# Optimization experiments

Hardware: AMD Instinct MI355X
Metric: run time of the kernel (lower is better)

The kernel has to match this reference:

```python
import jax, jax.numpy as jnp
import numpy as np

D_MODEL = 1024
NUM_HEADS = 16
ROPE_THETA = 10000.0


def setup_inputs() -> dict:
    key = jax.random.key(0)
    ks = jax.random.split(key, 5)
    B, S, D = 4, 2048, D_MODEL
    std = (2.0 / (D * D)) ** 0.5
    return {
        "x": jax.random.normal(ks[0], (B, S, D), dtype=jnp.float32),
        "Wq": jax.random.normal(ks[1], (D, D), dtype=jnp.float32) * std,
        "Wk": jax.random.normal(ks[2], (D, D), dtype=jnp.float32) * std,
        "Wv": jax.random.normal(ks[3], (D, D), dtype=jnp.float32) * std,
        "Wo": jax.random.normal(ks[4], (D, D), dtype=jnp.float32) * std,
    }


def _apply_rope(t, sin, cos):
    # t: [B, H, S, d_k]; sin/cos: [S, d_k//2] (broadcast over B, H)
    e = t[..., 0::2]
    o = t[..., 1::2]
    rot = jnp.stack((e * cos - o * sin, e * sin + o * cos), axis=-1)
    return rot.reshape(t.shape)  # interleave back to d_k


def reference(x, Wq, Wk, Wv, Wo):
    B, S, D = x.shape
    H = NUM_HEADS
    dk = D // H

    def proj(W):
        y = jnp.einsum('bsd,ed->bse', x, W)  # Linear: weight is [out, in]
        return y.reshape(B, S, H, dk).transpose(0, 2, 1, 3)  # [B,H,S,dk]

    q, k, v = proj(Wq), proj(Wk), proj(Wv)

    # RoPE cache (token_positions = arange(S))
    half = dk // 2
    inv_freq = 1.0 / (ROPE_THETA ** (jnp.arange(half, dtype=jnp.float32) * 2.0 / dk))
    angles = jnp.arange(S, dtype=jnp.float32)[:, None] * inv_freq[None, :]  # [S, half]
    sin, cos = jnp.sin(angles), jnp.cos(angles)
    q = _apply_rope(q, sin, cos)
    k = _apply_rope(k, sin, cos)

    # scaled dot-product attention with causal mask
    scores = jnp.einsum('bhqd,bhkd->bhqk', q, k) / jnp.sqrt(jnp.float32(dk))
    causal = jnp.tril(jnp.ones((S, S), dtype=bool))
    scores = jnp.where(causal, scores, jnp.finfo(scores.dtype).min)
    p = jax.nn.softmax(scores, axis=-1)
    out = jnp.einsum('bhqk,bhkd->bhqd', p, v)  # [B,H,S,dk]

    out = out.transpose(0, 2, 1, 3).reshape(B, S, D)
    return jnp.einsum('bsd,ed->bse', out, Wo)
```

## Files before the change

kernel.cpp:

```cpp
#include <hip/hip_runtime.h>

typedef unsigned short u16;
typedef unsigned int   u32;

typedef short    short8 __attribute__((ext_vector_type(8)));
typedef __bf16   bf16x8 __attribute__((ext_vector_type(8)));
typedef _Float16 half8  __attribute__((ext_vector_type(8)));
typedef float    f32x4  __attribute__((ext_vector_type(4)));

#define S_LEN   2048
#define DM      1024
#define NHEAD   16
#define DK      64
#define BH_TOT  64
#define M_TOK   8192
#define KDIM    1024

__device__ __forceinline__ u16 f2bf(float f) {
    u32 u = __builtin_bit_cast(u32, f);
    u += 0x7FFFu + ((u >> 16) & 1u);
    return (u16)(u >> 16);
}
__device__ __forceinline__ f32x4 mfma_bf16(short8 a, short8 b, f32x4 c) {
    return __builtin_amdgcn_mfma_f32_16x16x32_bf16(
        __builtin_bit_cast(bf16x8, a), __builtin_bit_cast(bf16x8, b), c, 0, 0, 0);
}
__device__ __forceinline__ f32x4 mfma_f16(half8 a, half8 b, f32x4 c) {
    return __builtin_amdgcn_mfma_f32_16x16x32_f16(a, b, c, 0, 0, 0);
}
__device__ __forceinline__ u32 pk_f16(float a, float b) {
    return __builtin_bit_cast(u32, __builtin_amdgcn_cvt_pkrtz(a, b));
}
__device__ __forceinline__ void gl_lds16(const void* g, void* l) {
    __builtin_amdgcn_global_load_lds(
        (const __attribute__((address_space(1))) u32*)g,
        (__attribute__((address_space(3))) u32*)l, 16, 0, 0);
}
__device__ __forceinline__ void bar_raw() { asm volatile("s_barrier" ::: "memory"); }
__device__ __forceinline__ void wait_vm4() { asm volatile("s_waitcnt vmcnt(4)" ::: "memory"); }
__device__ __forceinline__ void wait_vm0() { asm volatile("s_waitcnt vmcnt(0)" ::: "memory"); }

__device__ __forceinline__ int perm_inv(int rc) {
    const int nt = rc >> 4, mid = (rc >> 2) & 3, r = rc & 3;
    return 32 * (nt >> 1) + 8 * mid + 4 * (nt & 1) + r;
}

__global__ void cvt_all(const float4* __restrict__ x,  const float4* __restrict__ Wq,
                        const float4* __restrict__ Wk, const float4* __restrict__ Wv,
                        const float4* __restrict__ Wo,
                        uint2* __restrict__ oX, uint2* __restrict__ oWcat,
                        uint2* __restrict__ oWo,
                        float* __restrict__ sT, float* __restrict__ cT) {
    const int i = blockIdx.x * 256 + threadIdx.x;
    if (i < 3145728) {
        const float4* in;
        uint2* out;
        if (i < 2097152) {
            in = x + i;  out = oX + i;
        } else {
            const int j = i - 2097152;
            const int w = j >> 18, k = j & 262143;
            in  = (w == 0 ? Wq : w == 1 ? Wk : w == 2 ? Wv : Wo) + k;
            out = (w < 3) ? (oWcat + w * 262144 + k) : (oWo + k);
        }
        float4 f = *in;
        uint2 o;
        o.x = (u32)f2bf(f.x) | ((u32)f2bf(f.y) << 16);
        o.y = (u32)f2bf(f.z) | ((u32)f2bf(f.w) << 16);
        *out = o;
    } else {
        const int idx = i - 3145728;
        const float fi = expf(-(float)(idx >> 11) * 0.287823136624255f);
        const float ang = (float)(idx & 2047) * fi;
        sT[idx] = sinf(ang);
        cT[idx] = cosf(ang);
    }
}

template <int MODE>
__global__ __launch_bounds__(256)
void gemm_nt(const u16* __restrict__ A, const u16* __restrict__ Bw,
             u16* __restrict__ oQ, u16* __restrict__ oK, u16* __restrict__ oVt,
             float* __restrict__ oF,
             const float* __restrict__ ropeS, const float* __restrict__ ropeC) {
    __shared__ u16 As[2][128 * 32];
    __shared__ u16 Bs[2][128 * 32];
    const int tid  = threadIdx.x;
    const int wave = tid >> 6, lane = tid & 63;
    const int quad = lane >> 4, l15 = lane & 15;
    const int wr = wave >> 1, wc = wave & 1;
    const int NX  = (MODE == 0) ? 24 : 8;
    const int lin = (int)blockIdx.x + NX * (int)blockIdx.y;
    const int xcd = lin & 7, idx = lin >> 3;
    const int mbase = (xcd * 8 + idx / NX) * 128;
    const int nbase = (idx % NX) * 128;

    f32x4 acc[4][4];
#pragma unroll
    for (int i = 0; i < 4; i++)
#pragma unroll
        for (int j = 0; j < 4; j++) acc[i][j] = (f32x4)0.0f;

    const int srow0 = wave * 32 + (lane >> 2);
    const int srow1 = srow0 + 16;
    const int scolb = ((lane & 3) ^ ((lane >> 3) & 3)) * 16;
    const int ldsOff = wave * 2048 + lane * 16;
    const u16* gA0 = A  + (size_t)(mbase + srow0) * KDIM;
    const u16* gA1 = A  + (size_t)(mbase + srow1) * KDIM;
    const u16* gB0 = Bw + (size_t)(nbase + srow0) * KDIM;
    const u16* gB1 = Bw + (size_t)(nbase + srow1) * KDIM;
    const int koffq = (quad ^ ((l15 >> 1) & 3)) * 8;

    gl_lds16((const char*)gA0 + scolb, (char*)As[0] + ldsOff);
    gl_lds16((const char*)gA1 + scolb, (char*)As[0] + ldsOff + 1024);
    gl_lds16((const char*)gB0 + scolb, (char*)Bs[0] + ldsOff);
    gl_lds16((const char*)gB1 + scolb, (char*)Bs[0] + ldsOff + 1024);

    const int KT = KDIM / 32;
    for (int kt = 0; kt < KT; kt++) {
        const int cur = kt & 1, nxt = cur ^ 1;
        const int kkn = ((kt + 1 < KT) ? (kt + 1) : kt) * 32;
        bar_raw();
        gl_lds16((const char*)(gA0 + kkn) + scolb, (char*)As[nxt] + ldsOff);
        gl_lds16((const char*)(gA1 + kkn) + scolb, (char*)As[nxt] + ldsOff + 1024);
        gl_lds16((const char*)(gB0 + kkn) + scolb, (char*)Bs[nxt] + ldsOff);
        gl_lds16((const char*)(gB1 + kkn) + scolb, (char*)Bs[nxt] + ldsOff + 1024);
        wait_vm4();
        bar_raw();

        short8 af[4], bf[4];
#pragma unroll
        for (int mt = 0; mt < 4; mt++)
            af[mt] = *(const short8*)&As[cur][(wr * 64 + mt * 16 + l15) * 32 + koffq];
#pragma unroll
        for (int nt = 0; nt < 4; nt++)
            bf[nt] = *(const short8*)&Bs[cur][(wc * 64 + nt * 16 + l15) * 32 + koffq];
#pragma unroll
        for (int mt = 0; mt < 4; mt++)
#pragma unroll
            for (int nt = 0; nt < 4; nt++)
                acc[mt][nt] = mfma_bf16(af[mt], bf[nt], acc[mt][nt]);
    }
    wait_vm0();

    const int proj_blk = (MODE == 0) ? (nbase >> 10) : 2;

    const float* sB[4];
    const float* cB[4];
    if (MODE == 0 && proj_blk < 2) {
#pragma unroll
        for (int nt = 0; nt < 4; nt++) {
            const int fi = nt * 8 + (l15 >> 1);
            sB[nt] = ropeS + fi * 2048;
            cB[nt] = ropeC + fi * 2048;
        }
    }
    const int par = l15 & 1;

#pragma unroll
    for (int mt = 0; mt < 4; mt++) {
#pragma unroll
        for (int nt = 0; nt < 4; nt++) {
            const int n  = nbase + wc * 64 + nt * 16 + l15;
            const int mb = mbase + wr * 64 + mt * 16 + quad * 4;
            f32x4 v = acc[mt][nt];
            if (MODE == 0) {
                const int e = n & 1023;
                const int h = e >> 6, d = e & 63;
                if (proj_blk == 2) {
                    const int b_ = mb >> 11, s = mb & 2047;
                    const int bh = b_ * NHEAD + h;
                    uint2 pk;
                    pk.x = pk_f16(v[0], v[1]);
                    pk.y = pk_f16(v[2], v[3]);
                    *(uint2*)&oVt[((size_t)bh * DK + d) * S_LEN + s] = pk;
                } else {
                    u16* dst = (proj_blk == 0) ? oQ : oK;
                    float vp[4];
#pragma unroll
                    for (int r = 0; r < 4; r++) vp[r] = __shfl_xor(v[r], 1);
                    const int b_ = mb >> 11, s0 = mb & 2047;
                    const int bh = b_ * NHEAD + h;
                    const f32x4 sn = *(const f32x4*)(sB[nt] + s0);
                    const f32x4 cs = *(const f32x4*)(cB[nt] + s0);
#pragma unroll
                    for (int r = 0; r < 4; r++) {
                        const float res = par ? (vp[r] * sn[r] + v[r] * cs[r])
                                              : (v[r] * cs[r] - vp[r] * sn[r]);
                        dst[((size_t)bh * S_LEN + (s0 + r)) * DK + d] = f2bf(res);
                    }
                }
            } else {
#pragma unroll
                for (int r = 0; r < 4; r++)
                    oF[(size_t)(mb + r) * DM + n] = v[r];
            }
        }
    }
}

__global__ __launch_bounds__(256)
void flash_attn(const u16* __restrict__ Q, const u16* __restrict__ K,
                const u16* __restrict__ Vt, u16* __restrict__ Oc) {
    __shared__ u16 Ks[2][64 * 64];
    __shared__ u16 Vs[2][64 * 64];
    const int lin = (int)blockIdx.x + 64 * (int)blockIdx.y;
    const int xcd = lin & 7, idx = lin >> 3;
    const int bh  = xcd * 8 + (idx & 7);
    const int qt  = 15 - (idx >> 3);
    const int tid  = threadIdx.x;
    const int wave = tid >> 6, lane = tid & 63;
    const int quad = lane >> 4, l15 = lane & 15;
    const int x7 = l15 & 7;
    const size_t headQK = (size_t)bh * S_LEN * DK;
    const size_t headVt = (size_t)bh * DK * S_LEN;
    const int b = bh >> 4, h = bh & 15;
    const float SCL = 0.18033688011112042f;

    half8 ones;
#pragma unroll
    for (int j = 0; j < 8; j++) ones[j] = (_Float16)1.0f;

    const int rwl  = lane >> 3;
    const int scol = (lane & 7) ^ rwl;
    const int rc0 = wave * 16 + rwl, rc1 = rc0 + 8;
    const u16* gK0 = K  + headQK + (size_t)perm_inv(rc0) * DK + scol * 8;
    const u16* gK1 = K  + headQK + (size_t)perm_inv(rc1) * DK + scol * 8;
    const u16* gV0 = Vt + headVt + (size_t)rc0 * S_LEN + scol * 8;
    const u16* gV1 = Vt + headVt + (size_t)rc1 * S_LEN + scol * 8;
    const int ldsOff = wave * 2048 + lane * 16;
    const int koff0 = (quad ^ x7) * 8;
    const int koff1 = ((4 + quad) ^ x7) * 8;

    short8 qf[2][2];
#pragma unroll
    for (int hh = 0; hh < 2; hh++) {
        const int qrow = qt * 128 + hh * 64 + wave * 16 + l15;
        qf[hh][0] = *(const short8*)&Q[headQK + (size_t)qrow * DK + quad * 8];
        qf[hh][1] = *(const short8*)&Q[headQK + (size_t)qrow * DK + 32 + quad * 8];
    }

    float m_st[2];
    f32x4 lacc[2];
    f32x4 oacc[2][4];
#pragma unroll
    for (int hh = 0; hh < 2; hh++) {
        m_st[hh] = -__builtin_inff();
        lacc[hh] = (f32x4)0.0f;
#pragma unroll
        for (int n = 0; n < 4; n++) oacc[hh][n] = (f32x4)0.0f;
    }

    const int NT = 2 * qt + 2;
    gl_lds16(gK0, (char*)Ks[0] + ldsOff);
    gl_lds16(gK1, (char*)Ks[0] + ldsOff + 1024);
    gl_lds16(gV0, (char*)Vs[0] + ldsOff);
    gl_lds16(gV1, (char*)Vs[0] + ldsOff + 1024);

    for (int kt = 0; kt < NT; kt++) {
        const int cur = kt & 1, nxt = cur ^ 1;
        bar_raw();
        {
            const int ktn = (kt + 1 < NT) ? kt + 1 : kt;
            gl_lds16(gK0 + (size_t)ktn * 64 * DK, (char*)Ks[nxt] + ldsOff);
            gl_lds16(gK1 + (size_t)ktn * 64 * DK, (char*)Ks[nxt] + ldsOff + 1024);
            gl_lds16(gV0 + ktn * 64,              (char*)Vs[nxt] + ldsOff);
            gl_lds16(gV1 + ktn * 64,              (char*)Vs[nxt] + ldsOff + 1024);
        }
        wait_vm4();
        bar_raw();

#pragma unroll
        for (int hh = 0; hh < 2; hh++) {
            if (hh == 0 && kt == 2 * qt + 1) continue;
            f32x4 sc[4];
            __builtin_amdgcn_s_setprio(1);
#pragma unroll
            for (int nt = 0; nt < 4; nt++) {
                const int rb = (nt * 16 + l15) * 64;
                short8 kf0 = *(const short8*)&Ks[cur][rb + koff0];
                short8 kf1 = *(const short8*)&Ks[cur][rb + koff1];
                f32x4 z = (f32x4)0.0f;
                z = mfma_bf16(kf0, qf[hh][0], z);
                z = mfma_bf16(kf1, qf[hh][1], z);
#pragma unroll
                for (int r = 0; r < 4; r++) z[r] *= SCL;
                sc[nt] = z;
            }
            __builtin_amdgcn_s_setprio(0);
            if (kt == 2 * qt + hh) {
                const int qloc = wave * 16 + l15;
#pragma unroll
                for (int nt = 0; nt < 4; nt++) {
                    const int kb = 32 * (nt >> 1) + 8 * quad + 4 * (nt & 1);
#pragma unroll
                    for (int r = 0; r < 4; r++)
                        if (kb + r > qloc) sc[nt][r] = -__builtin_inff();
                }
            }
            float mx0 = fmaxf(fmaxf(sc[0][0], sc[0][1]), fmaxf(sc[0][2], sc[0][3]));
            float mx1 = fmaxf(fmaxf(sc[1][0], sc[1][1]), fmaxf(sc[1][2], sc[1][3]));
            float mx2 = fmaxf(fmaxf(sc[2][0], sc[2][1]), fmaxf(sc[2][2], sc[2][3]));
            float mx3 = fmaxf(fmaxf(sc[3][0], sc[3][1]), fmaxf(sc[3][2], sc[3][3]));
            float mx = fmaxf(fmaxf(mx0, mx1), fmaxf(mx2, mx3));
            mx = fmaxf(mx, __shfl_xor(mx, 16));
            mx = fmaxf(mx, __shfl_xor(mx, 32));
            const float mn = fmaxf(m_st[hh], mx);
            const float alpha = __builtin_amdgcn_exp2f(m_st[hh] - mn);
            m_st[hh] = mn;
#pragma unroll
            for (int nt = 0; nt < 4; nt++)
#pragma unroll
                for (int r = 0; r < 4; r++)
                    sc[nt][r] = __builtin_amdgcn_exp2f(sc[nt][r] - m_st[hh]);
            u32 pw[8];
            pw[0] = pk_f16(sc[0][0], sc[0][1]); pw[1] = pk_f16(sc[0][2], sc[0][3]);
            pw[2] = pk_f16(sc[1][0], sc[1][1]); pw[3] = pk_f16(sc[1][2], sc[1][3]);
            pw[4] = pk_f16(sc[2][0], sc[2][1]); pw[5] = pk_f16(sc[2][2], sc[2][3]);
            pw[6] = pk_f16(sc[3][0], sc[3][1]); pw[7] = pk_f16(sc[3][2], sc[3][3]);
            half8 pf0 = __builtin_bit_cast(half8, *(uint4*)&pw[0]);
            half8 pf1 = __builtin_bit_cast(half8, *(uint4*)&pw[4]);
            float alr[4];
#pragma unroll
            for (int r = 0; r < 4; r++) alr[r] = __shfl(alpha, quad * 20 + r);
#pragma unroll
            for (int n = 0; n < 4; n++)
#pragma unroll
                for (int r = 0; r < 4; r++) oacc[hh][n][r] *= alr[r];
#pragma unroll
            for (int r = 0; r < 4; r++) lacc[hh][r] *= alr[r];
            __builtin_amdgcn_s_setprio(1);
#pragma unroll
            for (int c = 0; c < 2; c++) {
                const half8 pf = c ? pf1 : pf0;
                lacc[hh] = mfma_f16(pf, ones, lacc[hh]);
                const int voff = ((c * 4 + quad) ^ x7) * 8;
#pragma unroll
                for (int nt2 = 0; nt2 < 4; nt2++) {
                    half8 vf = __builtin_bit_cast(half8,
                        *(const short8*)&Vs[cur][(nt2 * 16 + l15) * 64 + voff]);
                    oacc[hh][nt2] = mfma_f16(pf, vf, oacc[hh][nt2]);
                }
            }
            __builtin_amdgcn_s_setprio(0);
        }
    }
    wait_vm0();

#pragma unroll
    for (int hh = 0; hh < 2; hh++) {
#pragma unroll
        for (int r = 0; r < 4; r++) {
            const float inv = 1.0f / lacc[hh][r];
            const int s = qt * 128 + hh * 64 + wave * 16 + quad * 4 + r;
#pragma unroll
            for (int nt2 = 0; nt2 < 4; nt2++)
                Oc[((size_t)(b * S_LEN + s)) * DM + h * 64 + nt2 * 16 + l15] =
                    f2bf(oacc[hh][nt2][r] * inv);
        }
    }
}

#define OFF_XBF   ((size_t)0)
#define OFF_WCAT  ((size_t)8388608)
#define OFF_WO    ((size_t)11534336)
#define OFF_QB    ((size_t)12582912)
#define OFF_KB    ((size_t)20971520)
#define OFF_VT    ((size_t)29360128)
#define OFF_ROPE  ((size_t)37748736)

extern "C" void kernel_launch(void* const* d_in, const int* in_sizes, int n_in,
                              void* d_out, int out_size, void* d_ws, size_t ws_size,
                              hipStream_t stream) {
    const float* x  = (const float*)d_in[0];
    const float* Wq = (const float*)d_in[1];
    const float* Wk = (const float*)d_in[2];
    const float* Wv = (const float*)d_in[3];
    const float* Wo = (const float*)d_in[4];
    u16* ws  = (u16*)d_ws;
    u16* XBF = ws + OFF_XBF;
    u16* WCA = ws + OFF_WCAT;
    u16* WOB = ws + OFF_WO;
    u16* QB  = ws + OFF_QB;
    u16* KB  = ws + OFF_KB;
    u16* VT  = ws + OFF_VT;
    float* ropeS = (float*)(ws + OFF_ROPE);
    float* ropeC = ropeS + 65536;
    u16* AT  = XBF;

    cvt_all<<<12544, 256, 0, stream>>>((const float4*)x, (const float4*)Wq,
                                       (const float4*)Wk, (const float4*)Wv,
                                       (const float4*)Wo,
                                       (uint2*)XBF, (uint2*)WCA, (uint2*)WOB,
                                       ropeS, ropeC);

    gemm_nt<0><<<dim3(24, 64), 256, 0, stream>>>(XBF, WCA, QB, KB, VT, nullptr,
                                                 ropeS, ropeC);
    flash_attn<<<dim3(64, 16), 256, 0, stream>>>(QB, KB, VT, AT);
    gemm_nt<1><<<dim3(8, 64), 256, 0, stream>>>(AT, WOB, nullptr, nullptr, nullptr,
                                                (float*)d_out, nullptr, nullptr);
}
```

Baseline: 270.8 us.

## Halve attention query tile, add lazy softmax rescale, restructure GEMM K-loop

The flash attention kernel now handles one 64-row query tile per block instead of two, which doubles the grid to 2048 blocks, and it skips the online-softmax rescale unless the running max grows past a threshold. Scale multiplication moves into an FMA inside exp2. The GEMM K-loop now loads two 32-wide stages per iteration behind full __syncthreads, replacing the double-buffered prefetch. Smaller tiles add parallelism and shorten the causal tail, but K/V reuse per block halves and the GEMM loses its load/compute overlap.

```diff
diff --git a/kernel.cpp b/kernel.cpp
--- a/kernel.cpp
+++ b/kernel.cpp
@@ -12,8 +12,6 @@
 #define DM      1024
 #define NHEAD   16
 #define DK      64
-#define BH_TOT  64
-#define M_TOK   8192
 #define KDIM    1024
 
 __device__ __forceinline__ u16 f2bf(float f) {
@@ -111,37 +109,38 @@
     const u16* gB1 = Bw + (size_t)(nbase + srow1) * KDIM;
     const int koffq = (quad ^ ((l15 >> 1) & 3)) * 8;
 
-    gl_lds16((const char*)gA0 + scolb, (char*)As[0] + ldsOff);
-    gl_lds16((const char*)gA1 + scolb, (char*)As[0] + ldsOff + 1024);
-    gl_lds16((const char*)gB0 + scolb, (char*)Bs[0] + ldsOff);
-    gl_lds16((const char*)gB1 + scolb, (char*)Bs[0] + ldsOff + 1024);
-
-    const int KT = KDIM / 32;
+    const int KT = KDIM / 64;
     for (int kt = 0; kt < KT; kt++) {
-        const int cur = kt & 1, nxt = cur ^ 1;
-        const int kkn = ((kt + 1 < KT) ? (kt + 1) : kt) * 32;
-        bar_raw();
-        gl_lds16((const char*)(gA0 + kkn) + scolb, (char*)As[nxt] + ldsOff);
-        gl_lds16((const char*)(gA1 + kkn) + scolb, (char*)As[nxt] + ldsOff + 1024);
-        gl_lds16((const char*)(gB0 + kkn) + scolb, (char*)Bs[nxt] + ldsOff);
-        gl_lds16((const char*)(gB1 + kkn) + scolb, (char*)Bs[nxt] + ldsOff + 1024);
-        wait_vm4();
-        bar_raw();
-
-        short8 af[4], bf[4];
-#pragma unroll
-        for (int mt = 0; mt < 4; mt++)
-            af[mt] = *(const short8*)&As[cur][(wr * 64 + mt * 16 + l15) * 32 + koffq];
-#pragma unroll
-        for (int nt = 0; nt < 4; nt++)
-            bf[nt] = *(const short8*)&Bs[cur][(wc * 64 + nt * 16 + l15) * 32 + koffq];
-#pragma unroll
-        for (int mt = 0; mt < 4; mt++)
+        const int kk = kt * 64;
+        __syncthreads();
+#pragma unroll
+        for (int s = 0; s < 2; s++) {
+            const int ko = kk + s * 32;
+            gl_lds16((const char*)(gA0 + ko) + scolb, (char*)As[s] + ldsOff);
+            gl_lds16((const char*)(gA1 + ko) + scolb, (char*)As[s] + ldsOff + 1024);
+            gl_lds16((const char*)(gB0 + ko) + scolb, (char*)Bs[s] + ldsOff);
+            gl_lds16((const char*)(gB1 + ko) + scolb, (char*)Bs[s] + ldsOff + 1024);
+        }
+        __syncthreads();
+
+        short8 af[4][2], bf[4][2];
+#pragma unroll
+        for (int s = 0; s < 2; s++) {
+#pragma unroll
+            for (int mt = 0; mt < 4; mt++)
+                af[mt][s] = *(const short8*)&As[s][(wr * 64 + mt * 16 + l15) * 32 + koffq];
 #pragma unroll
             for (int nt = 0; nt < 4; nt++)
-                acc[mt][nt] = mfma_bf16(af[mt], bf[nt], acc[mt][nt]);
-    }
-    wait_vm0();
+                bf[nt][s] = *(const short8*)&Bs[s][(wc * 64 + nt * 16 + l15) * 32 + koffq];
+        }
+#pragma unroll
+        for (int s = 0; s < 2; s++)
+#pragma unroll
+            for (int mt = 0; mt < 4; mt++)
+#pragma unroll
+                for (int nt = 0; nt < 4; nt++)
+                    acc[mt][nt] = mfma_bf16(af[mt][s], bf[nt][s], acc[mt][nt]);
+    }
 
     const int proj_blk = (MODE == 0) ? (nbase >> 10) : 2;
 
@@ -207,7 +206,7 @@
     const int lin = (int)blockIdx.x + 64 * (int)blockIdx.y;
     const int xcd = lin & 7, idx = lin >> 3;
     const int bh  = xcd * 8 + (idx & 7);
-    const int qt  = 15 - (idx >> 3);
+    const int qt  = 31 - (idx >> 3);
     const int tid  = threadIdx.x;
     const int wave = tid >> 6, lane = tid & 63;
     const int quad = lane >> 4, l15 = lane & 15;
@@ -216,6 +215,7 @@
     const size_t headVt = (size_t)bh * DK * S_LEN;
     const int b = bh >> 4, h = bh & 15;
     const float SCL = 0.18033688011112042f;
+    const float THRESH = 44.3614195558365f;
 
     half8 ones;
 #pragma unroll
@@ -232,26 +232,20 @@
     const int koff0 = (quad ^ x7) * 8;
     const int koff1 = ((4 + quad) ^ x7) * 8;
 
-    short8 qf[2][2];
-#pragma unroll
-    for (int hh = 0; hh < 2; hh++) {
-        const int qrow = qt * 128 + hh * 64 + wave * 16 + l15;
-        qf[hh][0] = *(const short8*)&Q[headQK + (size_t)qrow * DK + quad * 8];
-        qf[hh][1] = *(const short8*)&Q[headQK + (size_t)qrow * DK + 32 + quad * 8];
-    }
-
-    float m_st[2];
-    f32x4 lacc[2];
-    f32x4 oacc[2][4];
-#pragma unroll
-    for (int hh = 0; hh < 2; hh++) {
-        m_st[hh] = -__builtin_inff();
-        lacc[hh] = (f32x4)0.0f;
-#pragma unroll
-        for (int n = 0; n < 4; n++) oacc[hh][n] = (f32x4)0.0f;
-    }
-
-    const int NT = 2 * qt + 2;
+    short8 qf0, qf1;
+    {
+        const int qrow = qt * 64 + wave * 16 + l15;
+        qf0 = *(const short8*)&Q[headQK + (size_t)qrow * DK + quad * 8];
+        qf1 = *(const short8*)&Q[headQK + (size_t)qrow * DK + 32 + quad * 8];
+    }
+
+    float m_st = -__builtin_inff();
+    f32x4 lacc = (f32x4)0.0f;
+    f32x4 oacc[4];
+#pragma unroll
+    for (int n = 0; n < 4; n++) oacc[n] = (f32x4)0.0f;
+
+    const int NT = qt + 1;
     gl_lds16(gK0, (char*)Ks[0] + ldsOff);
     gl_lds16(gK1, (char*)Ks[0] + ldsOff + 1024);
     gl_lds16(gV0, (char*)Vs[0] + ldsOff);
@@ -270,94 +264,91 @@
         wait_vm4();
         bar_raw();
 
-#pragma unroll
-        for (int hh = 0; hh < 2; hh++) {
-            if (hh == 0 && kt == 2 * qt + 1) continue;
-            f32x4 sc[4];
-            __builtin_amdgcn_s_setprio(1);
+        f32x4 sc[4];
+        __builtin_amdgcn_s_setprio(1);
+#pragma unroll
+        for (int nt = 0; nt < 4; nt++) {
+            const int rb = (nt * 16 + l15) * 64;
+            short8 kf0 = *(const short8*)&Ks[cur][rb + koff0];
+            short8 kf1 = *(const short8*)&Ks[cur][rb + koff1];
+            f32x4 z = (f32x4)0.0f;
+            z = mfma_bf16(kf0, qf0, z);
+            z = mfma_bf16(kf1, qf1, z);
+            sc[nt] = z;
+        }
+        __builtin_amdgcn_s_setprio(0);
+
+        if (kt == qt) {
+            const int qloc = wave * 16 + l15;
 #pragma unroll
             for (int nt = 0; nt < 4; nt++) {
-                const int rb = (nt * 16 + l15) * 64;
-                short8 kf0 = *(const short8*)&Ks[cur][rb + koff0];
-                short8 kf1 = *(const short8*)&Ks[cur][rb + koff1];
-                f32x4 z = (f32x4)0.0f;
-                z = mfma_bf16(kf0, qf[hh][0], z);
-                z = mfma_bf16(kf1, qf[hh][1], z);
-#pragma unroll
-                for (int r = 0; r < 4; r++) z[r] *= SCL;
-                sc[nt] = z;
+                const int kb = 32 * (nt >> 1) + 8 * quad + 4 * (nt & 1);
+#pragma unroll
+                for (int r = 0; r < 4; r++)
+                    if (kb + r > qloc) sc[nt][r] = -__builtin_inff();
             }
-            __builtin_amdgcn_s_setprio(0);
-            if (kt == 2 * qt + hh) {
-                const int qloc = wave * 16 + l15;
-#pragma unroll
-                for (int nt = 0; nt < 4; nt++) {
-                    const int kb = 32 * (nt >> 1) + 8 * quad + 4 * (nt & 1);
-#pragma unroll
-                    for (int r = 0; r < 4; r++)
-                        if (kb + r > qloc) sc[nt][r] = -__builtin_inff();
-                }
+        }
+        float mx0 = fmaxf(fmaxf(sc[0][0], sc[0][1]), fmaxf(sc[0][2], sc[0][3]));
+        float mx1 = fmaxf(fmaxf(sc[1][0], sc[1][1]), fmaxf(sc[1][2], sc[1][3]));
+        float mx2 = fmaxf(fmaxf(sc[2][0], sc[2][1]), fmaxf(sc[2][2], sc[2][3]));
+        float mx3 = fmaxf(fmaxf(sc[3][0], sc[3][1]), fmaxf(sc[3][2], sc[3][3]));
+        float mx = fmaxf(fmaxf(mx0, mx1), fmaxf(mx2, mx3));
+        mx = fmaxf(mx, __shfl_xor(mx, 16));
+        mx = fmaxf(mx, __shfl_xor(mx, 32));
+        if (!__all(mx - m_st <= THRESH)) {
+            const float mn = fmaxf(m_st, mx);
+            const float alpha = __builtin_amdgcn_exp2f((m_st - mn) * SCL);
+            m_st = mn;
+            float alr[4];
+#pragma unroll
+            for (int r = 0; r < 4; r++) alr[r] = __shfl(alpha, quad * 20 + r);
+#pragma unroll
+            for (int n = 0; n < 4; n++)
+#pragma unroll
+                for (int r = 0; r < 4; r++) oacc[n][r] *= alr[r];
+#pragma unroll
+            for (int r = 0; r < 4; r++) lacc[r] *= alr[r];
+        }
+        const float msc = m_st * SCL;
+#pragma unroll
+        for (int nt = 0; nt < 4; nt++)
+#pragma unroll
+            for (int r = 0; r < 4; r++)
+                sc[nt][r] = __builtin_amdgcn_exp2f(
+                    __builtin_fmaf(sc[nt][r], SCL, -msc));
+        u32 pw[8];
+        pw[0] = pk_f16(sc[0][0], sc[0][1]); pw[1] = pk_f16(sc[0][2], sc[0][3]);
+        pw[2] = pk_f16(sc[1][0], sc[1][1]); pw[3] = pk_f16(sc[1][2], sc[1][3]);
+        pw[4] = pk_f16(sc[2][0], sc[2][1]); pw[5] = pk_f16(sc[2][2], sc[2][3]);
+        pw[6] = pk_f16(sc[3][0], sc[3][1]); pw[7] = pk_f16(sc[3][2], sc[3][3]);
+        half8 pf0 = __builtin_bit_cast(half8, *(uint4*)&pw[0]);
+        half8 pf1 = __builtin_bit_cast(half8, *(uint4*)&pw[4]);
+
+        __builtin_amdgcn_s_setprio(1);
+#pragma unroll
+        for (int c = 0; c < 2; c++) {
+            const half8 pf = c ? pf1 : pf0;
+            lacc = mfma_f16(pf, ones, lacc);
+            const int voff = ((c * 4 + quad) ^ x7) * 8;
+#pragma unroll
+            for (int nt2 = 0; nt2 < 4; nt2++) {
+                half8 vf = __builtin_bit_cast(half8,
+                    *(const short8*)&Vs[cur][(nt2 * 16 + l15) * 64 + voff]);
+                oacc[nt2] = mfma_f16(pf, vf, oacc[nt2]);
             }
-            float mx0 = fmaxf(fmaxf(sc[0][0], sc[0][1]), fmaxf(sc[0][2], sc[0][3]));
-            float mx1 = fmaxf(fmaxf(sc[1][0], sc[1][1]), fmaxf(sc[1][2], sc[1][3]));
-            float mx2 = fmaxf(fmaxf(sc[2][0], sc[2][1]), fmaxf(sc[2][2], sc[2][3]));
-            float mx3 = fmaxf(fmaxf(sc[3][0], sc[3][1]), fmaxf(sc[3][2], sc[3][3]));
-            float mx = fmaxf(fmaxf(mx0, mx1), fmaxf(mx2, mx3));
-            mx = fmaxf(mx, __shfl_xor(mx, 16));
-            mx = fmaxf(mx, __shfl_xor(mx, 32));
-            const float mn = fmaxf(m_st[hh], mx);
-            const float alpha = __builtin_amdgcn_exp2f(m_st[hh] - mn);
-            m_st[hh] = mn;
-#pragma unroll
-            for (int nt = 0; nt < 4; nt++)
-#pragma unroll
-                for (int r = 0; r < 4; r++)
-                    sc[nt][r] = __builtin_amdgcn_exp2f(sc[nt][r] - m_st[hh]);
-            u32 pw[8];
-            pw[0] = pk_f16(sc[0][0], sc[0][1]); pw[1] = pk_f16(sc[0][2], sc[0][3]);
-            pw[2] = pk_f16(sc[1][0], sc[1][1]); pw[3] = pk_f16(sc[1][2], sc[1][3]);
-            pw[4] = pk_f16(sc[2][0], sc[2][1]); pw[5] = pk_f16(sc[2][2], sc[2][3]);
-            pw[6] = pk_f16(sc[3][0], sc[3][1]); pw[7] = pk_f16(sc[3][2], sc[3][3]);
-            half8 pf0 = __builtin_bit_cast(half8, *(uint4*)&pw[0]);
-            half8 pf1 = __builtin_bit_cast(half8, *(uint4*)&pw[4]);
-            float alr[4];
-#pragma unroll
-            for (int r = 0; r < 4; r++) alr[r] = __shfl(alpha, quad * 20 + r);
-#pragma unroll
-            for (int n = 0; n < 4; n++)
-#pragma unroll
-                for (int r = 0; r < 4; r++) oacc[hh][n][r] *= alr[r];
-#pragma unroll
-            for (int r = 0; r < 4; r++) lacc[hh][r] *= alr[r];
-            __builtin_amdgcn_s_setprio(1);
-#pragma unroll
-            for (int c = 0; c < 2; c++) {
-                const half8 pf = c ? pf1 : pf0;
-                lacc[hh] = mfma_f16(pf, ones, lacc[hh]);
-                const int voff = ((c * 4 + quad) ^ x7) * 8;
-#pragma unroll
-                for (int nt2 = 0; nt2 < 4; nt2++) {
-                    half8 vf = __builtin_bit_cast(half8,
-                        *(const short8*)&Vs[cur][(nt2 * 16 + l15) * 64 + voff]);
-                    oacc[hh][nt2] = mfma_f16(pf, vf, oacc[hh][nt2]);
-                }
-            }
-            __builtin_amdgcn_s_setprio(0);
-        }
+        }
+        __builtin_amdgcn_s_setprio(0);
     }
     wait_vm0();
 
 #pragma unroll
-    for (int hh = 0; hh < 2; hh++) {
-#pragma unroll
-        for (int r = 0; r < 4; r++) {
-            const float inv = 1.0f / lacc[hh][r];
-            const int s = qt * 128 + hh * 64 + wave * 16 + quad * 4 + r;
-#pragma unroll
-            for (int nt2 = 0; nt2 < 4; nt2++)
-                Oc[((size_t)(b * S_LEN + s)) * DM + h * 64 + nt2 * 16 + l15] =
-                    f2bf(oacc[hh][nt2][r] * inv);
-        }
+    for (int r = 0; r < 4; r++) {
+        const float inv = 1.0f / lacc[r];
+        const int s = qt * 64 + wave * 16 + quad * 4 + r;
+#pragma unroll
+        for (int nt2 = 0; nt2 < 4; nt2++)
+            Oc[((size_t)(b * S_LEN + s)) * DM + h * 64 + nt2 * 16 + l15] =
+                f2bf(oacc[nt2][r] * inv);
     }
 }
 
@@ -396,7 +387,7 @@
 
     gemm_nt<0><<<dim3(24, 64), 256, 0, stream>>>(XBF, WCA, QB, KB, VT, nullptr,
                                                  ropeS, ropeC);
-    flash_attn<<<dim3(64, 16), 256, 0, stream>>>(QB, KB, VT, AT);
+    flash_attn<<<dim3(64, 32), 256, 0, stream>>>(QB, KB, VT, AT);
     gemm_nt<1><<<dim3(8, 64), 256, 0, stream>>>(AT, WOB, nullptr, nullptr, nullptr,
                                                 (float*)d_out, nullptr, nullptr);
 }
```

After: 257.0 us. 5.1% less time.
